# Kernel optimization log

Measured on AMD Instinct MI355X. Metric: run time of the kernel, lower is better.

The kernel has to match this reference:

```python
import jax, jax.numpy as jnp
import numpy as np

B, C, H, W = 4, 256, 64, 64
R, KH, KW = 4, 3, 3
K = KH * KW  # 9 kernel taps


def _conv2d(x, w, b):
    # plain 3x3 conv, stride 1, pad 1, NCHW
    y = jax.lax.conv_general_dilated(x, w, (1, 1), ((1, 1), (1, 1)),
                                     dimension_numbers=('NCHW', 'OIHW', 'NCHW'))
    return y + b[None, :, None, None]


def _bilinear_sample(x, py, px):
    # x: [B,C,H,W]; py,px: [B,K,H,W] float coords; zero padding outside the image.
    B_, C_, H_, W_ = x.shape
    xf = x.reshape(B_, C_, H_ * W_)
    y0 = jnp.floor(py)
    x0 = jnp.floor(px)
    wy = py - y0
    wx = px - x0
    y0i = y0.astype(jnp.int32)
    x0i = x0.astype(jnp.int32)

    def corner(yi, xi, wgt):
        valid = (yi >= 0) & (yi < H_) & (xi >= 0) & (xi < W_)
        idx = (jnp.clip(yi, 0, H_ - 1) * W_ + jnp.clip(xi, 0, W_ - 1)).reshape(B_, -1)
        vals = jax.vmap(lambda xb, ib: jnp.take(xb, ib, axis=1))(xf, idx)  # [B,C,K*H*W]
        vals = vals.reshape(B_, C_, K, H_, W_)
        w_ = (wgt * valid).astype(x.dtype)[:, None]  # [B,1,K,H,W]
        return vals * w_

    out = corner(y0i, x0i, (1 - wy) * (1 - wx))
    out = out + corner(y0i, x0i + 1, (1 - wy) * wx)
    out = out + corner(y0i + 1, x0i, wy * (1 - wx))
    out = out + corner(y0i + 1, x0i + 1, wy * wx)
    return out  # [B,C,K,H,W]


def _deform_conv(x, offset, weight):
    # DCNv1: offset [B, 2K, H, W], interleaved (dy, dx) per kernel tap.
    B_, C_, H_, W_ = x.shape
    off = offset.reshape(B_, K, 2, H_, W_)
    ky, kx = jnp.meshgrid(jnp.arange(KH), jnp.arange(KW), indexing='ij')
    base_y = (ky.reshape(K) - (KH - 1) // 2).astype(x.dtype)
    base_x = (kx.reshape(K) - (KW - 1) // 2).astype(x.dtype)
    py = (jnp.arange(H_, dtype=x.dtype)[None, None, :, None]
          + base_y[None, :, None, None] + off[:, :, 0])
    px = (jnp.arange(W_, dtype=x.dtype)[None, None, None, :]
          + base_x[None, :, None, None] + off[:, :, 1])
    sampled = _bilinear_sample(x, py, px)  # [B,C,K,H,W]
    wr = weight.reshape(weight.shape[0], C_, K)
    return jnp.einsum('bckhw,ock->bohw', sampled, wr)


def setup_inputs() -> dict:
    key = jax.random.key(0)
    k1, k2, k3 = jax.random.split(key, 3)
    x = jax.random.normal(k1, (B, C, H, W), jnp.float32)
    off_w = jax.random.normal(k2, (R, 2 * K, C, KH, KW), jnp.float32) * 0.01
    off_b = jnp.zeros((R, 2 * K), jnp.float32)
    w = jax.random.normal(k3, (R, C, C, KH, KW), jnp.float32) * (1.0 / np.sqrt(C * K))
    return {"x": x, "off_w": off_w, "off_b": off_b, "w": w}


def reference(x, off_w, off_b, w):
    for r in range(R):  # fixed small layer count
        offset = _conv2d(x, off_w[r], off_b[r])
        x = jax.nn.relu(_deform_conv(x, offset, w[r]))
    return x
```

## Files before the change

### kernel.cpp

```cpp
#include <hip/hip_runtime.h>


#define HW 4096

typedef __attribute__((ext_vector_type(8))) __bf16 bf16x8;
typedef __attribute__((ext_vector_type(4))) float f32x4;
typedef __attribute__((ext_vector_type(8))) unsigned short u16x8;

__device__ inline unsigned int f2bf_bits(float f) {
  unsigned int u = __float_as_uint(f);
  return (u + 0x7fffu + ((u >> 16) & 1u)) >> 16;
}

__device__ inline void wg_barrier_lds() {
  asm volatile("s_waitcnt lgkmcnt(0)" ::: "memory");
  __builtin_amdgcn_s_barrier();
  __builtin_amdgcn_sched_barrier(0);
}

__global__ __launch_bounds__(256) void wpack_kernel(
    const float* __restrict__ w, unsigned short* __restrict__ wph) {
  const int f = blockIdx.x * 256 + threadIdx.x;
  const int j  = f & 7;
  const int l  = (f >> 3) & 63;
  const int nt = (f >> 9) & 15;
  const int q  = (f >> 13) % 72;
  const int r  = f / 589824;
  const int n  = nt * 16 + (l & 15);
  const int kk = q * 32 + ((l >> 4) << 3) + j;
  const int c  = kk & 255, k = kk >> 8;
  wph[f] = (unsigned short)f2bf_bits(w[((r * 256 + n) * 256 + c) * 9 + k]);
}

__global__ __launch_bounds__(256) void offwpack_kernel(
    const float* __restrict__ offw, unsigned short* __restrict__ owph) {
  const int f = blockIdx.x * 256 + threadIdx.x;
  const int j  = f & 7;
  const int l  = (f >> 3) & 63;
  const int nt = (f >> 9) & 1;
  const int q  = (f >> 10) % 72;
  const int r  = f / 73728;
  const int n  = nt * 16 + (l & 15);
  const int kk = q * 32 + ((l >> 4) << 3) + j;
  const int c  = kk & 255, k = kk >> 8;
  const float v = (n < 18) ? offw[((r * 18 + n) * 256 + c) * 9 + k] : 0.f;
  owph[f] = (unsigned short)f2bf_bits(v);
}

__global__ __launch_bounds__(256) void xpose_kernel(
    const float* __restrict__ x, unsigned short* __restrict__ xh) {
  const int p0 = blockIdx.x * 64;
  const int c0 = blockIdx.y * 64;
  const int b  = blockIdx.z;
  __shared__ float sT[64][65];
  const int t = threadIdx.x;
  const int pj = t & 63, ci0 = (t >> 6) * 16;
  const float* __restrict__ xb = x + ((size_t)(b * 256 + c0)) * HW + p0;
#pragma unroll
  for (int u = 0; u < 16; ++u)
    sT[ci0 + u][pj] = xb[(size_t)(ci0 + u) * HW + pj];
  __syncthreads();
  const int pr = t >> 2, cs = (t & 3) * 16;
  u16x8 va, vb;
#pragma unroll
  for (int u = 0; u < 8; ++u) va[u] = (unsigned short)f2bf_bits(sT[cs + u][pr]);
#pragma unroll
  for (int u = 0; u < 8; ++u) vb[u] = (unsigned short)f2bf_bits(sT[cs + 8 + u][pr]);
  const size_t o = ((size_t)b * HW + p0 + pr) * 256 + c0 + cs;
  *(u16x8*)(xh + o) = va;
  *(u16x8*)(xh + o + 8) = vb;
}

__global__ __launch_bounds__(1024, 4) void deform_mfma(
    const unsigned short* __restrict__ xh,
    const unsigned short* __restrict__ owh,
    const float* __restrict__ offb,
    const unsigned short* __restrict__ wph,
    unsigned short* __restrict__ yth,
    float* __restrict__ outf) {
  const int gid = blockIdx.x;
  const int b = (gid & 7) >> 1;
  const int h = ((gid >> 3) << 1) | (gid & 1);
  const int t = threadIdx.x, lane = t & 63, wv = t >> 6;
  const int frow = lane & 15, quad = lane >> 4;
  const int sm = t >> 4, cg = t & 15;

  __shared__ __align__(16) unsigned char smem[55808];
  float* s_cw = (float*)smem;
  int*   s_ci = (int*)(smem + 9216);
  unsigned char* sAb = smem + 18432;
  float* s_off = (float*)(smem + 51200);

  {
    const int kv = wv >> 3, ntO = (wv >> 2) & 1, mtO = wv & 3;
    const int mO = mtO * 16 + frow;
    f32x4 aoc = {0.f, 0.f, 0.f, 0.f};
    const u16x8 z8 = {};
    const size_t xb = (size_t)b * HW;
    const u16x8* __restrict__ owp = (const u16x8*)owh;

#define OHLOAD(k, p, A, Bv)                                                 \
  {                                                                         \
    const int ky = (k) / 3 - 1, kx = (k) % 3 - 1;                           \
    const int hy = h + ky;                                                  \
    const int hyc = hy < 0 ? 0 : (hy > 63 ? 63 : hy);                       \
    const int mx = mO + kx;                                                 \
    const bool v = ((unsigned)hy < 64u) && ((unsigned)mx < 64u);            \
    const int cpx = mx < 0 ? 0 : (mx > 63 ? 63 : mx);                       \
    const size_t abase = (xb + (size_t)(hyc * 64 + cpx)) * 256              \
                         + quad * 8 + kv * 128 + (p) * 64;                  \
    _Pragma("unroll") for (int j = 0; j < 2; ++j) {                         \
      A[j] = *(const u16x8*)(xh + abase + j * 32);                          \
      if (!v) A[j] = z8;                                                    \
    }                                                                       \
    _Pragma("unroll") for (int j = 0; j < 2; ++j)                           \
      Bv[j] = owp[(((k) * 8 + kv * 4 + (p) * 2 + j) * 2 + ntO) * 64 + lane];\
  }

#define OHMFMA(A, Bv)                                                       \
  _Pragma("unroll") for (int j = 0; j < 2; ++j)                             \
    aoc = __builtin_amdgcn_mfma_f32_16x16x32_bf16(                          \
        __builtin_bit_cast(bf16x8, A[j]), __builtin_bit_cast(bf16x8, Bv[j]),\
        aoc, 0, 0, 0);

    u16x8 A0[2], Bv0[2], A1[2], Bv1[2];
    OHLOAD(0, 0, A0, Bv0)
    OHLOAD(0, 1, A1, Bv1)
    OHMFMA(A0, Bv0) OHLOAD(1, 0, A0, Bv0)
    OHMFMA(A1, Bv1) OHLOAD(1, 1, A1, Bv1)
    OHMFMA(A0, Bv0) OHLOAD(2, 0, A0, Bv0)
    OHMFMA(A1, Bv1) OHLOAD(2, 1, A1, Bv1)
    OHMFMA(A0, Bv0) OHLOAD(3, 0, A0, Bv0)
    OHMFMA(A1, Bv1) OHLOAD(3, 1, A1, Bv1)
    OHMFMA(A0, Bv0) OHLOAD(4, 0, A0, Bv0)
    OHMFMA(A1, Bv1) OHLOAD(4, 1, A1, Bv1)
    OHMFMA(A0, Bv0) OHLOAD(5, 0, A0, Bv0)
    OHMFMA(A1, Bv1) OHLOAD(5, 1, A1, Bv1)
    OHMFMA(A0, Bv0) OHLOAD(6, 0, A0, Bv0)
    OHMFMA(A1, Bv1) OHLOAD(6, 1, A1, Bv1)
    OHMFMA(A0, Bv0) OHLOAD(7, 0, A0, Bv0)
    OHMFMA(A1, Bv1) OHLOAD(7, 1, A1, Bv1)
    OHMFMA(A0, Bv0) OHLOAD(8, 0, A0, Bv0)
    OHMFMA(A1, Bv1) OHLOAD(8, 1, A1, Bv1)
    OHMFMA(A0, Bv0)
    OHMFMA(A1, Bv1)
#undef OHLOAD
#undef OHMFMA

    f32x4* redp = (f32x4*)(smem + 18432);
    if (kv == 1) redp[(mtO * 2 + ntO) * 64 + lane] = aoc;
    __syncthreads();
    if (kv == 0) {
      const f32x4 o = redp[(mtO * 2 + ntO) * 64 + lane];
      aoc[0] += o[0]; aoc[1] += o[1]; aoc[2] += o[2]; aoc[3] += o[3];
      const int oc = ntO * 16 + frow;
      if (oc < 18) {
        const float bv = offb[oc];
        const int mb = mtO * 16 + quad * 4;
#pragma unroll
        for (int r = 0; r < 4; ++r) s_off[oc * 64 + mb + r] = aoc[r] + bv;
      }
    }
    __syncthreads();
  }

  if (t < 576) {
    const int k = t >> 6, m = t & 63;
    const int ky = k / 3 - 1, kx = k % 3 - 1;
    const float dy = s_off[(2 * k) * 64 + m];
    const float dx = s_off[(2 * k + 1) * 64 + m];
    const float py = (float)(h + ky) + dy;
    const float px = (float)(m + kx) + dx;
    const float y0f = floorf(py), x0f = floorf(px);
    const float wy = py - y0f, wx = px - x0f;
    const int y0 = (int)y0f, x0 = (int)x0f;
#pragma unroll
    for (int j = 0; j < 4; ++j) {
      const int yi = y0 + (j >> 1), xi = x0 + (j & 1);
      const bool v = (yi >= 0) && (yi < 64) && (xi >= 0) && (xi < 64);
      const float wgt = ((j >> 1) ? wy : 1.f - wy) * ((j & 1) ? wx : 1.f - wx);
      s_cw[(k * 4 + j) * 64 + m] = v ? wgt : 0.f;
      const int yc = yi < 0 ? 0 : (yi > 63 ? 63 : yi);
      const int xc = xi < 0 ? 0 : (xi > 63 ? 63 : xi);
      s_ci[(k * 4 + j) * 64 + m] = yc * 64 + xc;
    }
  }
  __syncthreads();

  f32x4 acc[2][2];
#pragma unroll
  for (int mt = 0; mt < 2; ++mt)
#pragma unroll
    for (int nt = 0; nt < 2; ++nt) acc[mt][nt] = (f32x4){0.f, 0.f, 0.f, 0.f};

  const char* __restrict__ xbc = (const char*)(xh + (size_t)b * HW * 256);
  const u16x8* __restrict__ wp = (const u16x8*)wph;
  const int bfo = (wv >> 1) * 2;
  const int mb0 = (wv & 1) << 5;

  const int gs = ((sm & 3) << 1) | ((sm >> 2) & 1);
  const int wbA = sm * 128 + ((((cg >> 2) ^ gs)) << 4) + (cg & 3) * 4;
  const int wbL = wbA ^ 64;
  const int gr = ((frow & 3) << 1) | ((frow >> 2) & 1);
  const int rb0 = (mb0 + frow) * 128 + ((quad ^ gr) << 4);
  const int rb1 = rb0 + 2048;

  unsigned int G0[4], G1[4];
  u16x8 B0[2], B1[2];
  float cwrC[4], cwrN[4];
  int cibC[4], cibN[4];
#pragma unroll
  for (int j = 0; j < 4; ++j) {
    cwrC[j] = s_cw[j * 64 + sm];
    cibC[j] = s_ci[j * 64 + sm] * 512;
  }
#pragma unroll
  for (int j = 0; j < 4; ++j)
    G0[j] = *(const unsigned int*)(xbc + cibC[j] + cg * 4);
#pragma unroll
  for (int j = 0; j < 4; ++j)
    G1[j] = *(const unsigned int*)(xbc + cibC[j] + 64 + cg * 4);
#pragma unroll
  for (int i = 0; i < 2; ++i) B0[i] = wp[(bfo + i) * 64 + lane];
#pragma unroll
  for (int i = 0; i < 2; ++i) B1[i] = wp[(16 + bfo + i) * 64 + lane];

#define COMBINE_STORE(Gx, BB)                                               \
  {                                                                         \
    float s0 = cwrC[0] * __uint_as_float(Gx[0] << 16);                      \
    float s1 = cwrC[0] * __uint_as_float(Gx[0] & 0xffff0000u);              \
    s0 = fmaf(cwrC[1], __uint_as_float(Gx[1] << 16), s0);                   \
    s1 = fmaf(cwrC[1], __uint_as_float(Gx[1] & 0xffff0000u), s1);           \
    s0 = fmaf(cwrC[2], __uint_as_float(Gx[2] << 16), s0);                   \
    s1 = fmaf(cwrC[2], __uint_as_float(Gx[2] & 0xffff0000u), s1);           \
    s0 = fmaf(cwrC[3], __uint_as_float(Gx[3] << 16), s0);                   \
    s1 = fmaf(cwrC[3], __uint_as_float(Gx[3] & 0xffff0000u), s1);           \
    const __bf16 hb0 = (__bf16)s0, hb1 = (__bf16)s1;                        \
    const unsigned int hv =                                                 \
        (unsigned int)__builtin_bit_cast(unsigned short, hb0) |             \
        ((unsigned int)__builtin_bit_cast(unsigned short, hb1) << 16);      \
    const float d0 = s0 - __uint_as_float(hv << 16);                        \
    const float d1 = s1 - __uint_as_float(hv & 0xffff0000u);                \
    const __bf16 lb0 = (__bf16)d0, lb1 = (__bf16)d1;                        \
    const unsigned int lv =                                                 \
        (unsigned int)__builtin_bit_cast(unsigned short, lb0) |             \
        ((unsigned int)__builtin_bit_cast(unsigned short, lb1) << 16);      \
    *(unsigned int*)(sAb + (BB) + wbA) = hv;                                \
    *(unsigned int*)(sAb + (BB) + wbL) = lv;                                \
  }

#define MFMA_BODY(BB, Bx)                                                   \
  {                                                                         \
    bf16x8 ah[2], al[2];                                                    \
    ah[0] = __builtin_bit_cast(bf16x8, *(const u16x8*)(sAb + (BB) + rb0));  \
    al[0] = __builtin_bit_cast(bf16x8,                                      \
                               *(const u16x8*)(sAb + (BB) + (rb0 ^ 64)));   \
    ah[1] = __builtin_bit_cast(bf16x8, *(const u16x8*)(sAb + (BB) + rb1));  \
    al[1] = __builtin_bit_cast(bf16x8,                                      \
                               *(const u16x8*)(sAb + (BB) + (rb1 ^ 64)));   \
    __builtin_amdgcn_s_setprio(1);                                          \
    _Pragma("unroll") for (int nt = 0; nt < 2; ++nt) {                      \
      const bf16x8 bv = __builtin_bit_cast(bf16x8, Bx[nt]);                 \
      _Pragma("unroll") for (int mt = 0; mt < 2; ++mt) {                    \
        acc[mt][nt] = __builtin_amdgcn_mfma_f32_16x16x32_bf16(              \
            ah[mt], bv, acc[mt][nt], 0, 0, 0);                              \
        acc[mt][nt] = __builtin_amdgcn_mfma_f32_16x16x32_bf16(              \
            al[mt], bv, acc[mt][nt], 0, 0, 0);                              \
      }                                                                     \
    }                                                                       \
    __builtin_amdgcn_s_setprio(0);                                          \
  }

  for (int k9 = 0; k9 < 9; ++k9) {
#pragma unroll
    for (int sp = 0; sp < 4; ++sp) {
      const int PB = (sp & 1) * 16384;
      COMBINE_STORE(G0, PB)
      COMBINE_STORE(G1, PB + 8192)
      wg_barrier_lds();
      const bool more = (k9 < 8) || (sp < 3);
      if (more) {
        if (sp == 3) {
#pragma unroll
          for (int j = 0; j < 4; ++j) {
            cwrN[j] = s_cw[((k9 + 1) * 4 + j) * 64 + sm];
            cibN[j] = s_ci[((k9 + 1) * 4 + j) * 64 + sm] * 512;
          }
#pragma unroll
          for (int j = 0; j < 4; ++j)
            G0[j] = *(const unsigned int*)(xbc + cibN[j] + cg * 4);
#pragma unroll
          for (int j = 0; j < 4; ++j)
            G1[j] = *(const unsigned int*)(xbc + cibN[j] + 64 + cg * 4);
        } else {
          const int c0b = ((2 * sp + 2) & 7) * 64 + cg * 4;
#pragma unroll
          for (int j = 0; j < 4; ++j)
            G0[j] = *(const unsigned int*)(xbc + cibC[j] + c0b);
#pragma unroll
          for (int j = 0; j < 4; ++j)
            G1[j] = *(const unsigned int*)(xbc + cibC[j] + c0b + 64);
        }
      }
      MFMA_BODY(PB, B0)
      if (more) {
        const int cn0 = k9 * 8 + 2 * sp + 2;
#pragma unroll
        for (int i = 0; i < 2; ++i)
          B0[i] = wp[(cn0 * 16 + bfo + i) * 64 + lane];
      }
      MFMA_BODY(PB + 8192, B1)
      if (more) {
        const int cn1 = k9 * 8 + 2 * sp + 3;
#pragma unroll
        for (int i = 0; i < 2; ++i)
          B1[i] = wp[(cn1 * 16 + bfo + i) * 64 + lane];
      }
      if (sp == 3 && k9 < 8) {
#pragma unroll
        for (int j = 0; j < 4; ++j) { cwrC[j] = cwrN[j]; cibC[j] = cibN[j]; }
      }
    }
  }
#undef COMBINE_STORE
#undef MFMA_BODY

  if (outf) {
#pragma unroll
    for (int mt = 0; mt < 2; ++mt)
#pragma unroll
      for (int nt = 0; nt < 2; ++nt) {
        const int n = (wv >> 1) * 32 + nt * 16 + frow;
        const int pos = h * 64 + mb0 + mt * 16 + quad * 4;
        float4 vv;
        vv.x = fmaxf(acc[mt][nt][0], 0.f);
        vv.y = fmaxf(acc[mt][nt][1], 0.f);
        vv.z = fmaxf(acc[mt][nt][2], 0.f);
        vv.w = fmaxf(acc[mt][nt][3], 0.f);
        *(float4*)&outf[(size_t)(b * 256 + n) * HW + pos] = vv;
      }
  } else {
    __syncthreads();
    unsigned short* sW = (unsigned short*)smem + wv * (32 * 36);
#pragma unroll
    for (int mt = 0; mt < 2; ++mt)
#pragma unroll
      for (int nt = 0; nt < 2; ++nt)
#pragma unroll
        for (int r = 0; r < 4; ++r)
          sW[(mt * 16 + quad * 4 + r) * 36 + nt * 16 + frow] =
              (unsigned short)f2bf_bits(fmaxf(acc[mt][nt][r], 0.f));
    __syncthreads();
    const int lm = lane & 31, cg2 = lane >> 5;
    const int pos = h * 64 + mb0 + lm;
    unsigned short* __restrict__ yp =
        yth + ((size_t)b * HW + pos) * 256 + (wv >> 1) * 32 + cg2 * 16;
#pragma unroll
    for (int g = 0; g < 2; ++g)
      *(u16x8*)(yp + g * 8) = *(const u16x8*)&sW[lm * 36 + cg2 * 16 + g * 8];
  }
}

extern "C" void kernel_launch(void* const* d_in, const int* in_sizes, int n_in,
                              void* d_out, int out_size, void* d_ws, size_t ws_size,
                              hipStream_t stream) {
  const float* x0   = (const float*)d_in[0];
  const float* offw = (const float*)d_in[1];
  const float* offb = (const float*)d_in[2];
  const float* w    = (const float*)d_in[3];
  float* out = (float*)d_out;
  float* ws  = (float*)d_ws;

  unsigned short* wph  = (unsigned short*)(ws + 294912);
  unsigned short* owph = wph + 2359296;
  unsigned short* xTA  = owph + 294912;
  unsigned short* xTB  = xTA + 4194304;

  wpack_kernel<<<9216, 256, 0, stream>>>(w, wph);
  offwpack_kernel<<<1152, 256, 0, stream>>>(offw, owph);
  xpose_kernel<<<dim3(64, 4, 4), 256, 0, stream>>>(x0, xTA);

  unsigned short* pin = xTA;
  unsigned short* pout = xTB;
  for (int r = 0; r < 4; ++r) {
    deform_mfma<<<256, 1024, 0, stream>>>(pin, owph + r * 73728,
                                          offb + r * 18,
                                          wph + (size_t)r * 589824,
                                          (r < 3) ? pout : nullptr,
                                          (r < 3) ? nullptr : out);
    unsigned short* tmp = pin; pin = pout; pout = tmp;
  }
}
```

Measured before the change: 337.6 us.

## Split K across wave halves with 64-wide N tiles and LDS reduction

Reorganizes the wave-to-tile mapping so each wave computes a 32x64 output tile (four N subtiles) and the two channel sub-blocks per step are split between wave groups (split-K). This raises the A-fragment reuse per LDS read and halves the B loads per MFMA per wave. The partial sums are then reduced through LDS in two phases before the epilogue. The cost is extra accumulator registers, extra barriers and reduction traffic at the end, and it appears to assume 16 waves per block, which the launch code would need to match.

```diff
diff --git a/kernel.cpp b/kernel.cpp
--- a/kernel.cpp
+++ b/kernel.cpp
@@ -187,26 +187,28 @@
   }
   __syncthreads();
 
-  f32x4 acc[2][2];
+  f32x4 acc[2][4];
 #pragma unroll
   for (int mt = 0; mt < 2; ++mt)
 #pragma unroll
-    for (int nt = 0; nt < 2; ++nt) acc[mt][nt] = (f32x4){0.f, 0.f, 0.f, 0.f};
+    for (int nt = 0; nt < 4; ++nt) acc[mt][nt] = (f32x4){0.f, 0.f, 0.f, 0.f};
 
   const char* __restrict__ xbc = (const char*)(xh + (size_t)b * HW * 256);
   const u16x8* __restrict__ wp = (const u16x8*)wph;
-  const int bfo = (wv >> 1) * 2;
-  const int mb0 = (wv & 1) << 5;
+  const int kv  = wv >> 3;
+  const int wmh = (wv >> 2) & 1;
+  const int wng = wv & 3;
+  const int bfo = wng * 4;
 
   const int gs = ((sm & 3) << 1) | ((sm >> 2) & 1);
   const int wbA = sm * 128 + ((((cg >> 2) ^ gs)) << 4) + (cg & 3) * 4;
   const int wbL = wbA ^ 64;
   const int gr = ((frow & 3) << 1) | ((frow >> 2) & 1);
-  const int rb0 = (mb0 + frow) * 128 + ((quad ^ gr) << 4);
+  const int rb0 = (wmh * 32 + frow) * 128 + ((quad ^ gr) << 4) + kv * 8192;
   const int rb1 = rb0 + 2048;
 
   unsigned int G0[4], G1[4];
-  u16x8 B0[2], B1[2];
+  u16x8 Bc[4], Bn[4];
   float cwrC[4], cwrN[4];
   int cibC[4], cibN[4];
 #pragma unroll
@@ -221,9 +223,8 @@
   for (int j = 0; j < 4; ++j)
     G1[j] = *(const unsigned int*)(xbc + cibC[j] + 64 + cg * 4);
 #pragma unroll
-  for (int i = 0; i < 2; ++i) B0[i] = wp[(bfo + i) * 64 + lane];
-#pragma unroll
-  for (int i = 0; i < 2; ++i) B1[i] = wp[(16 + bfo + i) * 64 + lane];
+  for (int i = 0; i < 4; ++i)
+    Bc[i] = wp[(kv * 16 + bfo + i) * 64 + lane];
 
 #define COMBINE_STORE(Gx, BB)                                               \
   {                                                                         \
@@ -249,18 +250,18 @@
     *(unsigned int*)(sAb + (BB) + wbL) = lv;                                \
   }
 
-#define MFMA_BODY(BB, Bx)                                                   \
+#define MFMA_BODY(PBv)                                                      \
   {                                                                         \
     bf16x8 ah[2], al[2];                                                    \
-    ah[0] = __builtin_bit_cast(bf16x8, *(const u16x8*)(sAb + (BB) + rb0));  \
+    ah[0] = __builtin_bit_cast(bf16x8, *(const u16x8*)(sAb + (PBv) + rb0)); \
     al[0] = __builtin_bit_cast(bf16x8,                                      \
-                               *(const u16x8*)(sAb + (BB) + (rb0 ^ 64)));   \
-    ah[1] = __builtin_bit_cast(bf16x8, *(const u16x8*)(sAb + (BB) + rb1));  \
+                               *(const u16x8*)(sAb + (PBv) + (rb0 ^ 64)));  \
+    ah[1] = __builtin_bit_cast(bf16x8, *(const u16x8*)(sAb + (PBv) + rb1)); \
     al[1] = __builtin_bit_cast(bf16x8,                                      \
-                               *(const u16x8*)(sAb + (BB) + (rb1 ^ 64)));   \
+                               *(const u16x8*)(sAb + (PBv) + (rb1 ^ 64)));  \
     __builtin_amdgcn_s_setprio(1);                                          \
-    _Pragma("unroll") for (int nt = 0; nt < 2; ++nt) {                      \
-      const bf16x8 bv = __builtin_bit_cast(bf16x8, Bx[nt]);                 \
+    _Pragma("unroll") for (int nt = 0; nt < 4; ++nt) {                      \
+      const bf16x8 bv = __builtin_bit_cast(bf16x8, Bc[nt]);                 \
       _Pragma("unroll") for (int mt = 0; mt < 2; ++mt) {                    \
         acc[mt][nt] = __builtin_amdgcn_mfma_f32_16x16x32_bf16(              \
             ah[mt], bv, acc[mt][nt], 0, 0, 0);                              \
@@ -302,19 +303,14 @@
             G1[j] = *(const unsigned int*)(xbc + cibC[j] + c0b + 64);
         }
       }
-      MFMA_BODY(PB, B0)
+      MFMA_BODY(PB)
       if (more) {
-        const int cn0 = k9 * 8 + 2 * sp + 2;
-#pragma unroll
-        for (int i = 0; i < 2; ++i)
-          B0[i] = wp[(cn0 * 16 + bfo + i) * 64 + lane];
-      }
-      MFMA_BODY(PB + 8192, B1)
-      if (more) {
-        const int cn1 = k9 * 8 + 2 * sp + 3;
-#pragma unroll
-        for (int i = 0; i < 2; ++i)
-          B1[i] = wp[(cn1 * 16 + bfo + i) * 64 + lane];
+        const int cn = k9 * 8 + 2 * sp + kv + 2;
+#pragma unroll
+        for (int i = 0; i < 4; ++i)
+          Bn[i] = wp[(cn * 16 + bfo + i) * 64 + lane];
+#pragma unroll
+        for (int i = 0; i < 4; ++i) Bc[i] = Bn[i];
       }
       if (sp == 3 && k9 < 8) {
 #pragma unroll
@@ -325,39 +321,74 @@
 #undef COMBINE_STORE
 #undef MFMA_BODY
 
+  __syncthreads();
+  {
+    float* redb = (float*)sAb;
+    const int rbase = ((wv & 7) * 64 + lane) * 16;
+#pragma unroll
+    for (int ph = 0; ph < 2; ++ph) {
+      if (kv == 1) {
+#pragma unroll
+        for (int mt = 0; mt < 2; ++mt)
+#pragma unroll
+          for (int q2 = 0; q2 < 2; ++q2)
+            *(f32x4*)&redb[rbase + (mt * 2 + q2) * 4] = acc[mt][ph * 2 + q2];
+      }
+      __syncthreads();
+      if (kv == 0) {
+#pragma unroll
+        for (int mt = 0; mt < 2; ++mt)
+#pragma unroll
+          for (int q2 = 0; q2 < 2; ++q2) {
+            const f32x4 o = *(const f32x4*)&redb[rbase + (mt * 2 + q2) * 4];
+            acc[mt][ph * 2 + q2][0] += o[0];
+            acc[mt][ph * 2 + q2][1] += o[1];
+            acc[mt][ph * 2 + q2][2] += o[2];
+            acc[mt][ph * 2 + q2][3] += o[3];
+          }
+      }
+      __syncthreads();
+    }
+  }
+
   if (outf) {
-#pragma unroll
-    for (int mt = 0; mt < 2; ++mt)
-#pragma unroll
-      for (int nt = 0; nt < 2; ++nt) {
-        const int n = (wv >> 1) * 32 + nt * 16 + frow;
-        const int pos = h * 64 + mb0 + mt * 16 + quad * 4;
-        float4 vv;
-        vv.x = fmaxf(acc[mt][nt][0], 0.f);
-        vv.y = fmaxf(acc[mt][nt][1], 0.f);
-        vv.z = fmaxf(acc[mt][nt][2], 0.f);
-        vv.w = fmaxf(acc[mt][nt][3], 0.f);
-        *(float4*)&outf[(size_t)(b * 256 + n) * HW + pos] = vv;
-      }
+    if (kv == 0) {
+#pragma unroll
+      for (int mt = 0; mt < 2; ++mt)
+#pragma unroll
+        for (int nt = 0; nt < 4; ++nt) {
+          const int n = wng * 64 + nt * 16 + frow;
+          const int pos = h * 64 + wmh * 32 + mt * 16 + quad * 4;
+          float4 vv;
+          vv.x = fmaxf(acc[mt][nt][0], 0.f);
+          vv.y = fmaxf(acc[mt][nt][1], 0.f);
+          vv.z = fmaxf(acc[mt][nt][2], 0.f);
+          vv.w = fmaxf(acc[mt][nt][3], 0.f);
+          *(float4*)&outf[(size_t)(b * 256 + n) * HW + pos] = vv;
+        }
+    }
   } else {
+    unsigned short* sW = (unsigned short*)(smem + (wv & 7) * 4608);
+    if (kv == 0) {
+#pragma unroll
+      for (int mt = 0; mt < 2; ++mt)
+#pragma unroll
+        for (int nt = 0; nt < 4; ++nt)
+#pragma unroll
+          for (int r = 0; r < 4; ++r)
+            sW[(mt * 16 + quad * 4 + r) * 72 + nt * 16 + frow] =
+                (unsigned short)f2bf_bits(fmaxf(acc[mt][nt][r], 0.f));
+    }
     __syncthreads();
-    unsigned short* sW = (unsigned short*)smem + wv * (32 * 36);
-#pragma unroll
-    for (int mt = 0; mt < 2; ++mt)
-#pragma unroll
-      for (int nt = 0; nt < 2; ++nt)
-#pragma unroll
-        for (int r = 0; r < 4; ++r)
-          sW[(mt * 16 + quad * 4 + r) * 36 + nt * 16 + frow] =
-              (unsigned short)f2bf_bits(fmaxf(acc[mt][nt][r], 0.f));
-    __syncthreads();
-    const int lm = lane & 31, cg2 = lane >> 5;
-    const int pos = h * 64 + mb0 + lm;
-    unsigned short* __restrict__ yp =
-        yth + ((size_t)b * HW + pos) * 256 + (wv >> 1) * 32 + cg2 * 16;
-#pragma unroll
-    for (int g = 0; g < 2; ++g)
-      *(u16x8*)(yp + g * 8) = *(const u16x8*)&sW[lm * 36 + cg2 * 16 + g * 8];
+    if (kv == 0) {
+      const int rowl = lane & 31, colh = lane >> 5;
+      const int pos = h * 64 + wmh * 32 + rowl;
+      unsigned short* __restrict__ yp =
+          yth + ((size_t)b * HW + pos) * 256 + wng * 64 + colh * 32;
+#pragma unroll
+      for (int g = 0; g < 4; ++g)
+        *(u16x8*)(yp + g * 8) = *(const u16x8*)&sW[rowl * 72 + colh * 32 + g * 8];
+    }
   }
 }
 
```

After: 345.6 us. +2.4%, slower.
